# Performance work log

Hardware: AMD Instinct MI355X
Metric: run time of the kernel (lower is better)

## Reference

```python
import jax, jax.numpy as jnp
import numpy as np

N = 25000      # nodes per type
E = 300000     # weight-edge rows
K = 16         # neighbors
F = 64         # in_feat
A = 64         # atten_dim
DW = 64        # weight_dim
CB = 8         # num_bit_conv
CV = 8         # num_vector_conv
OUT = 64       # out_feat
IN_K = CB * F + CV * (3 + 2 + 1)


def setup_inputs() -> dict:
    key = jax.random.key(0)
    ks = jax.random.split(key, 40)
    s = 0.05
    d = {}
    d['eu'] = jax.random.normal(ks[0], (N, F), jnp.float32)
    d['ei'] = jax.random.normal(ks[1], (N, F), jnp.float32)
    d['et'] = jax.random.normal(ks[2], (N, F), jnp.float32)
    d['ew'] = jax.random.normal(ks[3], (E, DW), jnp.float32)
    names = ['u_iw_j', 'u_tw_j', 'i_uw_j', 'i_tw_j', 't_uw_j', 't_iw_j']
    for i, nm in enumerate(names):
        d[nm] = jax.random.randint(ks[4 + i], (N, K), 0, N, jnp.int64 if jax.config.jax_enable_x64 else jnp.int32)
        d[nm.replace('_j', '_w')] = jax.random.randint(ks[10 + i], (N, K), 0, E, jnp.int64 if jax.config.jax_enable_x64 else jnp.int32)
    # per-type Attention1 params: user, item, tag
    for i, t in enumerate(['user', 'item', 'tag']):
        b = 16 + 4 * i
        d[f'W1_{t}'] = jax.random.normal(ks[b], (F + DW, A), jnp.float32) * s
        d[f'W2_{t}'] = jax.random.normal(ks[b + 1], (F, A), jnp.float32) * s
        d[f'b_{t}'] = jax.random.normal(ks[b + 2], (1, A), jnp.float32) * s
        d[f'v_{t}'] = jax.random.normal(ks[b + 3], (1, A), jnp.float32) * s
    d['U'] = jax.random.normal(ks[28], (F, A), jnp.float32) * s
    d['q'] = jax.random.normal(ks[29], (1, A), jnp.float32) * s
    d['p'] = jax.random.normal(ks[30], (1, A), jnp.float32) * s
    d['W_bit'] = jax.random.normal(ks[31], (CB, 3), jnp.float32) * s       # Conv2d(1,CB,(3,1))
    d['W_vec1'] = jax.random.normal(ks[32], (CV, 1, F), jnp.float32) * s   # Conv2d(1,CV,(1,F))
    d['W_vec2'] = jax.random.normal(ks[33], (CV, 2, F), jnp.float32) * s
    d['W_vec3'] = jax.random.normal(ks[34], (CV, 3, F), jnp.float32) * s
    d['Wf'] = jax.random.normal(ks[35], (IN_K, OUT), jnp.float32) * s
    d['bf'] = jax.random.normal(ks[36], (1, OUT), jnp.float32) * s
    return d


def _atten1(ev, ej, ew, v_j, v_w, W1, W2, b, v):
    ejp = jnp.concatenate([jnp.zeros((1, ej.shape[1]), ej.dtype), ej], axis=0)
    ewp = jnp.concatenate([jnp.zeros((1, ew.shape[1]), ew.dtype), ew], axis=0)
    eNj = ejp[v_j]                                  # [N,K,F]
    eNw = ewp[v_w]                                  # [N,K,DW]
    eNv = jnp.broadcast_to(ev[:, None, :], (ev.shape[0], v_j.shape[1], ev.shape[1]))
    eN_vw = jnp.concatenate([eNv, eNw], axis=-1)    # [N,K,F+DW]
    av = jnp.einsum('nkd,da->nka', eN_vw, W1) + jnp.einsum('nkf,fa->nka', eNj, W2) + b
    x = jax.nn.relu(av) @ v.T                       # [N,K,1]
    a = jax.nn.softmax(x, axis=1)
    return jnp.sum(a * eNj, axis=1)                 # [N,F]


def _atten2(u, i, t, U, q, p):
    uit = jnp.stack([u, i, t], axis=1)              # [N,3,F]
    x = jnp.einsum('nsf,fa->nsa', uit, U) + q
    x = jax.nn.relu(x) @ p.T                        # [N,3,1]
    b = jax.nn.softmax(x, axis=1)
    return b * uit                                  # [N,3,F]


def _conv(eN, W_bit, W_vec1, W_vec2, W_vec3):
    # eN: [N,3,F]
    bit = jax.nn.relu(jnp.einsum('njf,cj->ncf', eN, W_bit))       # [N,CB,F]
    bit = bit.reshape(bit.shape[0], -1)
    vec = []
    for j, W in ((1, W_vec1), (2, W_vec2), (3, W_vec3)):
        win = jnp.stack([eN[:, s:s + j, :] for s in range(3 - j + 1)], axis=1)  # [N,4-j,j,F]
        y = jax.nn.relu(jnp.einsum('nsjf,cjf->ncs', win, W))       # [N,CV,4-j]
        vec.append(y.reshape(y.shape[0], -1))
    return jnp.concatenate([bit] + vec, axis=1)                    # [N,IN_K]


def _forward(eu, ei, et, ew, params, idx):
    (W1u, W2u, bu, vu, W1i, W2i, bi, vi, W1t, W2t, bt, vt,
     U, q, p, W_bit, W_vec1, W_vec2, W_vec3, Wf, bf) = params
    (u_iw_j, u_iw_w, u_tw_j, u_tw_w, i_uw_j, i_uw_w,
     i_tw_j, i_tw_w, t_uw_j, t_uw_w, t_iw_j, t_iw_w) = idx
    eu_iN = _atten1(eu, ei, ew, u_iw_j, u_iw_w, W1i, W2i, bi, vi)
    eu_tN = _atten1(eu, et, ew, u_tw_j, u_tw_w, W1t, W2t, bt, vt)
    ei_uN = _atten1(ei, eu, ew, i_uw_j, i_uw_w, W1u, W2u, bu, vu)
    ei_tN = _atten1(ei, et, ew, i_tw_j, i_tw_w, W1t, W2t, bt, vt)
    et_uN = _atten1(et, eu, ew, t_uw_j, t_uw_w, W1u, W2u, bu, vu)
    et_iN = _atten1(et, ei, ew, t_iw_j, t_iw_w, W1i, W2i, bi, vi)
    euN = _atten2(eu, eu_iN, eu_tN, U, q, p)
    eiN = _atten2(ei_uN, ei, ei_tN, U, q, p)
    etN = _atten2(et_uN, et_iN, et, U, q, p)
    out = []
    for eN in (euN, eiN, etN):
        c = _conv(eN, W_bit, W_vec1, W_vec2, W_vec3)
        out.append(jax.nn.relu(c @ Wf + bf))
    return tuple(out)


def reference(eu, ei, et, ew,
              u_iw_j, u_iw_w, u_tw_j, u_tw_w, i_uw_j, i_uw_w, i_tw_j, i_tw_w,
              t_uw_j, t_uw_w, t_iw_j, t_iw_w,
              W1_user, W2_user, b_user, v_user,
              W1_item, W2_item, b_item, v_item,
              W1_tag, W2_tag, b_tag, v_tag,
              U, q, p, W_bit, W_vec1, W_vec2, W_vec3, Wf, bf):
    params = (W1_user, W2_user, b_user, v_user, W1_item, W2_item, b_item, v_item,
              W1_tag, W2_tag, b_tag, v_tag, U, q, p, W_bit, W_vec1, W_vec2, W_vec3, Wf, bf)
    idx = (u_iw_j, u_iw_w, u_tw_j, u_tw_w, i_uw_j, i_uw_w,
           i_tw_j, i_tw_w, t_uw_j, t_uw_w, t_iw_j, t_iw_w)
    return _forward(eu, ei, et, ew, params, idx)
```

## Files before the change

### kernel.cpp

```cpp
#include <hip/hip_runtime.h>
#include <math.h>

#define NN 25000
#define EE 300000
#define NT 1563
#define ET128 2344
#define NT128 196

typedef __attribute__((ext_vector_type(8))) short bf16x8;
typedef __attribute__((ext_vector_type(4))) float f32x4;
typedef __attribute__((ext_vector_type(2))) float f32x2;
typedef __attribute__((ext_vector_type(2))) __fp16 h2;

__device__ __forceinline__ unsigned short f2bf(float f) {
    union { float f; unsigned u; } a; a.f = f;
    unsigned r = (a.u + 0x7fffu + ((a.u >> 16) & 1u)) >> 16;
    return (unsigned short)r;
}
__device__ __forceinline__ unsigned pack2(float lo, float hi) {
    return (unsigned)f2bf(lo) | ((unsigned)f2bf(hi) << 16);
}
__device__ __forceinline__ float bflo(unsigned p) {
    union { unsigned u; float f; } a; a.u = p << 16; return a.f;
}
__device__ __forceinline__ float bfhi(unsigned p) {
    union { unsigned u; float f; } a; a.u = p & 0xffff0000u; return a.f;
}
__device__ __forceinline__ unsigned packfp8x4(float a, float b, float c, float d) {
    int v = __builtin_amdgcn_cvt_pk_fp8_f32(a, b, 0, 0);
    v = __builtin_amdgcn_cvt_pk_fp8_f32(c, d, v, 1);
    return (unsigned)v;
}
__device__ __forceinline__ unsigned pkh(float lo, float hi) {
    h2 r = __builtin_amdgcn_cvt_pkrtz(lo, hi);
    return __builtin_bit_cast(unsigned, r);
}
template<bool HI>
__device__ __forceinline__ h2 fp8toh(unsigned v) {
#if __has_builtin(__builtin_amdgcn_cvt_scalef32_pk_f16_fp8)
    return __builtin_amdgcn_cvt_scalef32_pk_f16_fp8((int)v, 1.0f, HI);
#else
    f32x2 f = __builtin_amdgcn_cvt_pk_f32_fp8((int)v, HI);
    return __builtin_amdgcn_cvt_pkrtz(f.x, f.y);
#endif
}
__device__ __forceinline__ float hdot(h2 a, h2 b, float c) {
#if __has_builtin(__builtin_amdgcn_fdot2)
    return __builtin_amdgcn_fdot2(a, b, c, false);
#else
    return c + (float)a[0] * (float)b[0] + (float)a[1] * (float)b[1];
#endif
}
__device__ __forceinline__ h2 hmax0(h2 a) {
    h2 z; z[0] = (__fp16)0.f; z[1] = (__fp16)0.f;
#if __has_builtin(__builtin_elementwise_max)
    return __builtin_elementwise_max(a, z);
#else
    h2 r;
    r[0] = a[0] > z[0] ? a[0] : z[0];
    r[1] = a[1] > z[1] ? a[1] : z[1];
    return r;
#endif
}

__global__ __launch_bounds__(256) void head_kernel(
    const float* __restrict__ ew,
    const float* __restrict__ eu, const float* __restrict__ ei, const float* __restrict__ et,
    const float* __restrict__ W1u, const float* __restrict__ W1i, const float* __restrict__ W1t,
    const float* __restrict__ W2u, const float* __restrict__ W2i, const float* __restrict__ W2t,
    const float* __restrict__ bu, const float* __restrict__ bi, const float* __restrict__ bt,
    unsigned char* __restrict__ gw8, unsigned* __restrict__ preB,
    unsigned char* __restrict__ JG)
{
    __shared__ __align__(16) unsigned short stA[64 * 72];
    __shared__ __align__(16) float cSa[64 * 68];
    __shared__ __align__(16) float cSb[64 * 68];
    const int t = threadIdx.x;
    const int lane = t & 63, wv = t >> 6;
    const int l15 = lane & 15, quad = lane >> 4;
    const int cw = wv * 16 + l15;
    const int bx = blockIdx.x;

    if (bx < ET128) {
        if (bx == 0 && t < 48) {
            int w = t >> 4;
            ((unsigned*)(gw8 + (size_t)w * (EE + 1) * 64))[t & 15] = 0u;
        }
        const float* Ws[3] = { W1u + 4096, W1i + 4096, W1t + 4096 };
        bf16x8 bf[3][2];
        #pragma unroll
        for (int w = 0; w < 3; ++w)
            #pragma unroll
            for (int ks = 0; ks < 2; ++ks)
                #pragma unroll
                for (int j = 0; j < 8; ++j)
                    bf[w][ks][j] = (short)f2bf(Ws[w][(ks * 32 + quad * 8 + j) * 64 + cw]);

        #pragma unroll
        for (int tile = 0; tile < 2; ++tile) {
            const int rowBase = bx * 128 + tile * 64;
            #pragma unroll
            for (int i = 0; i < 4; ++i) {
                int idx = t + i * 256;
                int row = idx >> 4, cg = idx & 15;
                int gr = rowBase + row;
                float4 v4 = (gr < EE) ? *(const float4*)(ew + (size_t)gr * 64 + cg * 4)
                                      : make_float4(0.f, 0.f, 0.f, 0.f);
                uint2 pk = { pack2(v4.x, v4.y), pack2(v4.z, v4.w) };
                *(uint2*)&stA[row * 72 + cg * 4] = pk;
            }
            __syncthreads();
            bf16x8 af[4][2];
            #pragma unroll
            for (int m = 0; m < 4; ++m)
                #pragma unroll
                for (int ks = 0; ks < 2; ++ks)
                    af[m][ks] = *(const bf16x8*)&stA[(m * 16 + l15) * 72 + ks * 32 + quad * 8];

            f32x4 acc[3][4];
            #pragma unroll
            for (int w = 0; w < 3; ++w)
                #pragma unroll
                for (int m = 0; m < 4; ++m) {
                    acc[w][m].x = 0; acc[w][m].y = 0; acc[w][m].z = 0; acc[w][m].w = 0;
                    #pragma unroll
                    for (int ks = 0; ks < 2; ++ks)
                        acc[w][m] = __builtin_amdgcn_mfma_f32_16x16x32_bf16(af[m][ks], bf[w][ks], acc[w][m], 0, 0, 0);
                }

            #define EG_WRITE(BUF, W) {                                               \
                _Pragma("unroll")                                                    \
                for (int m = 0; m < 4; ++m)                                          \
                    _Pragma("unroll")                                                \
                    for (int r = 0; r < 4; ++r)                                      \
                        BUF[(m * 16 + quad * 4 + r) * 68 + cw] = acc[W][m][r];       \
            }
            #define EG_STORE(BUF, W) {                                               \
                unsigned char* outg = gw8 + (size_t)(W) * (EE + 1) * 64 + 64;        \
                _Pragma("unroll")                                                    \
                for (int i = 0; i < 2; ++i) {                                        \
                    int task = t + i * 256;                                          \
                    int row = task >> 3, seg = task & 7;                             \
                    int gr = rowBase + row;                                          \
                    if (gr < EE) {                                                   \
                        float4 a = *(const float4*)&BUF[row * 68 + seg * 8];         \
                        float4 b = *(const float4*)&BUF[row * 68 + seg * 8 + 4];     \
                        uint2 pk = { packfp8x4(a.x, a.y, a.z, a.w),                  \
                                     packfp8x4(b.x, b.y, b.z, b.w) };                \
                        *(uint2*)(outg + (size_t)gr * 64 + seg * 8) = pk;            \
                    }                                                                \
                }                                                                    \
            }
            EG_WRITE(cSa, 0);
            __syncthreads();
            EG_STORE(cSa, 0);
            EG_WRITE(cSb, 1);
            __syncthreads();
            EG_STORE(cSb, 1);
            EG_WRITE(cSa, 2);
            __syncthreads();
            EG_STORE(cSa, 2);
            #undef EG_WRITE
            #undef EG_STORE
        }
    } else {
        const int yy = bx - ET128;
        const int y = yy / NT128;
        const int rowBase0 = (yy - y * NT128) * 128;
        if (rowBase0 == 0 && t < 48)
            ((unsigned*)(JG + (size_t)y * (NN + 1) * 192))[t] = 0u;
        const float* X; const float* Wa; const float* Wb; const float* W2;
        const float* ba; const float* bb; int oa, ob;
        switch (y) {
            case 0:  X = eu; Wa = W1i; ba = bi; oa = 0; Wb = W1t; bb = bt; ob = 1; W2 = W2u; break;
            case 1:  X = ei; Wa = W1u; ba = bu; oa = 2; Wb = W1t; bb = bt; ob = 3; W2 = W2i; break;
            default: X = et; Wa = W1u; ba = bu; oa = 4; Wb = W1i; bb = bi; ob = 5; W2 = W2t; break;
        }
        const float* Ws[3] = { Wa, Wb, W2 };
        const float bias_cw[3] = { ba[cw], bb[cw], 0.f };
        bf16x8 bf[3][2];
        #pragma unroll
        for (int w = 0; w < 3; ++w)
            #pragma unroll
            for (int ks = 0; ks < 2; ++ks)
                #pragma unroll
                for (int j = 0; j < 8; ++j)
                    bf[w][ks][j] = (short)f2bf(Ws[w][(ks * 32 + quad * 8 + j) * 64 + cw]);

        #pragma unroll
        for (int tile = 0; tile < 2; ++tile) {
            const int rowBase = rowBase0 + tile * 64;
            if (tile) __syncthreads();
            #pragma unroll
            for (int i = 0; i < 4; ++i) {
                int idx = t + i * 256;
                int row = idx >> 4, cg = idx & 15;
                int gr = rowBase + row;
                float4 v4 = (gr < NN) ? *(const float4*)(X + (size_t)gr * 64 + cg * 4)
                                      : make_float4(0.f, 0.f, 0.f, 0.f);
                uint2 pk = { pack2(v4.x, v4.y), pack2(v4.z, v4.w) };
                *(uint2*)&stA[row * 72 + cg * 4] = pk;
            }
            __syncthreads();
            bf16x8 af[4][2];
            #pragma unroll
            for (int m = 0; m < 4; ++m)
                #pragma unroll
                for (int ks = 0; ks < 2; ++ks)
                    af[m][ks] = *(const bf16x8*)&stA[(m * 16 + l15) * 72 + ks * 32 + quad * 8];

            f32x4 acc[3][4];
            #pragma unroll
            for (int w = 0; w < 3; ++w)
                #pragma unroll
                for (int m = 0; m < 4; ++m) {
                    acc[w][m].x = 0; acc[w][m].y = 0; acc[w][m].z = 0; acc[w][m].w = 0;
                    #pragma unroll
                    for (int ks = 0; ks < 2; ++ks)
                        acc[w][m] = __builtin_amdgcn_mfma_f32_16x16x32_bf16(af[m][ks], bf[w][ks], acc[w][m], 0, 0, 0);
                }

            #define NG_WRITE(BUF, W) {                                                     \
                _Pragma("unroll")                                                          \
                for (int m = 0; m < 4; ++m)                                                \
                    _Pragma("unroll")                                                      \
                    for (int r = 0; r < 4; ++r)                                            \
                        BUF[(m * 16 + quad * 4 + r) * 68 + cw] = acc[W][m][r] + bias_cw[W];\
            }
            #define NG_STORE(BUF, W) {                                                     \
                _Pragma("unroll")                                                          \
                for (int i = 0; i < 2; ++i) {                                              \
                    int task = t + i * 256;                                                \
                    int row = task >> 3, seg = task & 7;                                   \
                    int gr = rowBase + row;                                                \
                    if (gr < NN) {                                                         \
                        float4 a = *(const float4*)&BUF[row * 68 + seg * 8];               \
                        float4 b = *(const float4*)&BUF[row * 68 + seg * 8 + 4];           \
                        if ((W) < 2) {                                                     \
                            int oi = ((W) == 0) ? oa : ob;                                 \
                            uint4 pk = { pkh(a.x, a.y), pkh(a.z, a.w),                     \
                                         pkh(b.x, b.y), pkh(b.z, b.w) };                   \
                            *(uint4*)(preB + ((size_t)oi * NN + gr) * 32 + seg * 4) = pk;  \
                        } else {                                                           \
                            unsigned char* dst = JG + ((size_t)y * (NN + 1) + gr + 1) * 192;\
                            uint2 gj = { packfp8x4(a.x, a.y, a.z, a.w),                    \
                                         packfp8x4(b.x, b.y, b.z, b.w) };                  \
                            *(uint2*)(dst + seg * 8) = gj;                                 \
                            uint4 ej = *(const uint4*)&stA[row * 72 + seg * 8];            \
                            *(uint4*)(dst + 64 + seg * 16) = ej;                           \
                        }                                                                  \
                    }                                                                      \
                }                                                                          \
            }
            NG_WRITE(cSa, 0);
            __syncthreads();
            NG_STORE(cSa, 0);
            NG_WRITE(cSb, 1);
            __syncthreads();
            NG_STORE(cSb, 1);
            NG_WRITE(cSa, 2);
            __syncthreads();
            NG_STORE(cSa, 2);
            #undef NG_WRITE
            #undef NG_STORE
        }
    }
}

__global__ __launch_bounds__(256) void atten1_kernel(
    const unsigned* __restrict__ preB, const unsigned char* __restrict__ gw8,
    const unsigned char* __restrict__ JG,
    const float* __restrict__ vu, const float* __restrict__ vi, const float* __restrict__ vt,
    const int* __restrict__ u_iw_j, const int* __restrict__ u_iw_w,
    const int* __restrict__ u_tw_j, const int* __restrict__ u_tw_w,
    const int* __restrict__ i_uw_j, const int* __restrict__ i_uw_w,
    const int* __restrict__ i_tw_j, const int* __restrict__ i_tw_w,
    const int* __restrict__ t_uw_j, const int* __restrict__ t_uw_w,
    const int* __restrict__ t_iw_j, const int* __restrict__ t_iw_w,
    unsigned* __restrict__ aoB)
{
    const int g = blockIdx.y;
    const int p = blockIdx.x & 1;
    const int tile = blockIdx.x >> 1;
    int y; const int* Vj; const int* Vw;
    switch (g * 2 + p) {
        case 0:  y = 2; Vj = i_uw_j; Vw = i_uw_w; break;
        case 1:  y = 4; Vj = t_uw_j; Vw = t_uw_w; break;
        case 2:  y = 0; Vj = u_iw_j; Vw = u_iw_w; break;
        case 3:  y = 5; Vj = t_iw_j; Vw = t_iw_w; break;
        case 4:  y = 1; Vj = u_tw_j; Vw = u_tw_w; break;
        default: y = 3; Vj = i_tw_j; Vw = i_tw_w; break;
    }
    const float* v = (g == 0) ? vu : (g == 1) ? vi : vt;
    const unsigned* pre = preB + (size_t)y * NN * 32;
    const unsigned char* gw = gw8 + (size_t)g * (EE + 1) * 64;
    const unsigned char* jg = JG + (size_t)g * (NN + 1) * 192;
    unsigned*            out = aoB + (size_t)y * NN * 32;

    const int lane = threadIdx.x & 63;
    const int n = tile * 4 + (threadIdx.x >> 6);
    const int q = lane >> 4, r = lane & 15;

    const uint2 prep = *(const uint2*)(pre + (size_t)n * 32 + 2 * r);
    const h2 pre01 = __builtin_bit_cast(h2, prep.x);
    const h2 pre23 = __builtin_bit_cast(h2, prep.y);
    const float4 v4 = *(const float4*)(v + r * 4);
    const h2 v01h = __builtin_amdgcn_cvt_pkrtz(v4.x, v4.y);
    const h2 v23h = __builtin_amdgcn_cvt_pkrtz(v4.z, v4.w);

    const int4 wi = *(const int4*)(Vw + n * 16 + q * 4);
    const int4 ji = *(const int4*)(Vj + n * 16 + q * 4);
    const int wid[4] = { wi.x, wi.y, wi.z, wi.w };
    const int jid[4] = { ji.x, ji.y, ji.z, ji.w };

    unsigned gwv[4], gjv[4]; uint2 ejv[4];
    #pragma unroll
    for (int i = 0; i < 4; ++i)
        gwv[i] = *(const unsigned*)(gw + (size_t)wid[i] * 64 + r * 4);
    #pragma unroll
    for (int i = 0; i < 4; ++i) {
        const unsigned char* row = jg + (size_t)jid[i] * 192;
        gjv[i] = *(const unsigned*)(row + r * 4);
        ejv[i] = *(const uint2*)(row + 64 + r * 8);
    }

    float xk[4];
    #pragma unroll
    for (int i = 0; i < 4; ++i) {
        h2 g01 = fp8toh<false>(gwv[i]);
        h2 g23 = fp8toh<true>(gwv[i]);
        h2 j01 = fp8toh<false>(gjv[i]);
        h2 j23 = fp8toh<true>(gjv[i]);
        h2 z01 = hmax0(pre01 + g01 + j01);
        h2 z23 = hmax0(pre23 + g23 + j23);
        float x = hdot(z01, v01h, 0.f);
        x = hdot(z23, v23h, x);
        x += __shfl_xor(x, 1, 64);
        x += __shfl_xor(x, 2, 64);
        x += __shfl_xor(x, 4, 64);
        x += __shfl_xor(x, 8, 64);
        xk[i] = x;
    }
    float m = fmaxf(fmaxf(xk[0], xk[1]), fmaxf(xk[2], xk[3]));
    m = fmaxf(m, __shfl_xor(m, 16, 64));
    m = fmaxf(m, __shfl_xor(m, 32, 64));
    float e0 = __expf(xk[0] - m), e1 = __expf(xk[1] - m);
    float e2 = __expf(xk[2] - m), e3 = __expf(xk[3] - m);
    float s = (e0 + e1) + (e2 + e3);
    s += __shfl_xor(s, 16, 64);
    s += __shfl_xor(s, 32, 64);
    const float inv = 1.f / s;

    const float wgt[4] = { e0 * inv, e1 * inv, e2 * inv, e3 * inv };
    f32x2 A01; A01.x = 0.f; A01.y = 0.f;
    f32x2 A23; A23.x = 0.f; A23.y = 0.f;
    #pragma unroll
    for (int i = 0; i < 4; ++i) {
        f32x2 w2; w2.x = wgt[i]; w2.y = wgt[i];
        f32x2 e01; e01.x = bflo(ejv[i].x); e01.y = bfhi(ejv[i].x);
        f32x2 e23; e23.x = bflo(ejv[i].y); e23.y = bfhi(ejv[i].y);
        A01 = e01 * w2 + A01;
        A23 = e23 * w2 + A23;
    }
    float a0 = A01.x, a1 = A01.y, a2 = A23.x, a3 = A23.y;
    a0 += __shfl_xor(a0, 16, 64); a0 += __shfl_xor(a0, 32, 64);
    a1 += __shfl_xor(a1, 16, 64); a1 += __shfl_xor(a1, 32, 64);
    a2 += __shfl_xor(a2, 16, 64); a2 += __shfl_xor(a2, 32, 64);
    a3 += __shfl_xor(a3, 16, 64); a3 += __shfl_xor(a3, 32, 64);
    if (q == 0) {
        uint2 pk = { pack2(a0, a1), pack2(a2, a3) };
        *(uint2*)(out + (size_t)n * 32 + 2 * r) = pk;
    }
}

__global__ __launch_bounds__(256, 3) void tail_kernel(
    const float* __restrict__ eu, const float* __restrict__ ei, const float* __restrict__ et,
    const unsigned* __restrict__ aoB,
    const float* __restrict__ U, const float* __restrict__ q, const float* __restrict__ p,
    const float* __restrict__ Wbit, const float* __restrict__ Wv1,
    const float* __restrict__ Wv2, const float* __restrict__ Wv3,
    const float* __restrict__ Wf, const float* __restrict__ bfv,
    float* __restrict__ out)
{
    __shared__ __align__(16) unsigned short uitA[48 * 72];
    __shared__ __align__(16) unsigned short eNA[48 * 72];
    __shared__ __align__(16) unsigned short wcf[6 * 64 * 8];
    __shared__ __align__(16) unsigned short c_sh[16 * 584];
    __shared__ float G_sh[48 * 52];
    __shared__ float xpart[4 * 48];
    __shared__ float bcoef[16 * 4];

    const int t = threadIdx.x;
    const int lane = t & 63;
    const int wv = t >> 6;
    const int l15 = lane & 15;
    const int quad = lane >> 4;
    const int type = blockIdx.y;
    const float* xf = (type == 0) ? eu : (type == 1) ? ei : et;
    const int cw = wv * 16 + l15;
    const float qv = q[cw], pv = p[cw], bfb = bfv[cw];

    float wb[8][3];
    #pragma unroll
    for (int c = 0; c < 8; ++c)
        #pragma unroll
        for (int s = 0; s < 3; ++s) wb[c][s] = Wbit[c * 3 + s];

    bf16x8 ufrag[2];
    #pragma unroll
    for (int ks = 0; ks < 2; ++ks)
        #pragma unroll
        for (int j = 0; j < 8; ++j) {
            int f = ks * 32 + quad * 8 + j;
            ufrag[ks][j] = (short)f2bf(U[f * 64 + cw]);
        }
    bf16x8 wff[18];
    #pragma unroll
    for (int ks = 0; ks < 18; ++ks)
        #pragma unroll
        for (int j = 0; j < 8; ++j) {
            int k = ks * 32 + quad * 8 + j;
            float w = (k < 560) ? Wf[(size_t)k * 64 + cw] : 0.f;
            wff[ks][j] = (short)f2bf(w);
        }
    for (int slot = t; slot < 384; slot += 256) {
        int fi = slot >> 6, l = slot & 63;
        int nt_ = fi >> 1, ks = fi & 1;
        int r = nt_ * 16 + (l & 15);
        unsigned short vals[8];
        #pragma unroll
        for (int j = 0; j < 8; ++j) {
            int f = ks * 32 + (l >> 4) * 8 + j;
            float wv_;
            if (r < 8)       wv_ = Wv1[r * 64 + f];
            else if (r < 24) { int u = r - 8;  wv_ = Wv2[(u >> 1) * 128 + (u & 1) * 64 + f]; }
            else             { int u = r - 24; wv_ = Wv3[(u / 3) * 192 + (u % 3) * 64 + f]; }
            vals[j] = f2bf(wv_);
        }
        uint4 pk = { (unsigned)vals[0] | ((unsigned)vals[1] << 16),
                     (unsigned)vals[2] | ((unsigned)vals[3] << 16),
                     (unsigned)vals[4] | ((unsigned)vals[5] << 16),
                     (unsigned)vals[6] | ((unsigned)vals[7] << 16) };
        *(uint4*)&wcf[slot * 8] = pk;
    }

    for (int tile = blockIdx.x; tile < NT; tile += gridDim.x) {
        const int nodeBase = tile * 16;
        __syncthreads();
        #pragma unroll
        for (int i = 0; i < 3; ++i) {
            int idx = t + i * 256;
            int row = idx >> 4, cg = idx & 15;
            int nl = row / 3, s = row - nl * 3;
            int n = nodeBase + nl;
            uint2 pk;
            if (s == type) {
                float4 v4 = (n < NN) ? *(const float4*)(xf + (size_t)n * 64 + cg * 4)
                                     : make_float4(0.f, 0.f, 0.f, 0.f);
                pk.x = pack2(v4.x, v4.y); pk.y = pack2(v4.z, v4.w);
            } else {
                int aoidx = (type == 0) ? (s - 1)
                          : (type == 1) ? ((s == 0) ? 2 : 3)
                                        : ((s == 0) ? 4 : 5);
                pk = (n < NN) ? *(const uint2*)(aoB + ((size_t)aoidx * NN + n) * 32 + cg * 2)
                              : make_uint2(0u, 0u);
            }
            *(uint2*)&uitA[row * 72 + cg * 4] = pk;
        }
        __syncthreads();
        {
            f32x4 av[3];
            #pragma unroll
            for (int mt = 0; mt < 3; ++mt) { av[mt].x = 0; av[mt].y = 0; av[mt].z = 0; av[mt].w = 0; }
            #pragma unroll
            for (int mt = 0; mt < 3; ++mt)
                #pragma unroll
                for (int ks = 0; ks < 2; ++ks) {
                    bf16x8 a = *(const bf16x8*)&uitA[(mt * 16 + l15) * 72 + ks * 32 + quad * 8];
                    av[mt] = __builtin_amdgcn_mfma_f32_16x16x32_bf16(a, ufrag[ks], av[mt], 0, 0, 0);
                }
            #pragma unroll
            for (int mt = 0; mt < 3; ++mt)
                #pragma unroll
                for (int r = 0; r < 4; ++r) {
                    float val = fmaxf(av[mt][r] + qv, 0.f) * pv;
                    val += __shfl_xor(val, 1, 64); val += __shfl_xor(val, 2, 64);
                    val += __shfl_xor(val, 4, 64); val += __shfl_xor(val, 8, 64);
                    if (l15 == 0) xpart[wv * 48 + mt * 16 + quad * 4 + r] = val;
                }
        }
        __syncthreads();
        if (t < 16) {
            float xv[3];
            #pragma unroll
            for (int s = 0; s < 3; ++s)
                xv[s] = xpart[t * 3 + s] + xpart[48 + t * 3 + s]
                      + xpart[96 + t * 3 + s] + xpart[144 + t * 3 + s];
            float mm = fmaxf(xv[0], fmaxf(xv[1], xv[2]));
            float e0 = __expf(xv[0] - mm), e1 = __expf(xv[1] - mm), e2 = __expf(xv[2] - mm);
            float inv = 1.f / (e0 + e1 + e2);
            bcoef[t * 4 + 0] = e0 * inv; bcoef[t * 4 + 1] = e1 * inv; bcoef[t * 4 + 2] = e2 * inv;
        }
        __syncthreads();
        #pragma unroll
        for (int i = 0; i < 2; ++i) {
            int task = t + i * 256;
            int nl = task >> 5, fp = task & 31;
            float b0 = bcoef[nl * 4], b1 = bcoef[nl * 4 + 1], b2 = bcoef[nl * 4 + 2];
            unsigned u0 = *(const unsigned*)&uitA[(nl * 3 + 0) * 72 + fp * 2];
            unsigned u1 = *(const unsigned*)&uitA[(nl * 3 + 1) * 72 + fp * 2];
            unsigned u2 = *(const unsigned*)&uitA[(nl * 3 + 2) * 72 + fp * 2];
            float e0l = b0 * bflo(u0), e0h = b0 * bfhi(u0);
            float e1l = b1 * bflo(u1), e1h = b1 * bfhi(u1);
            float e2l = b2 * bflo(u2), e2h = b2 * bfhi(u2);
            *(unsigned*)&eNA[(nl * 3 + 0) * 72 + fp * 2] = pack2(e0l, e0h);
            *(unsigned*)&eNA[(nl * 3 + 1) * 72 + fp * 2] = pack2(e1l, e1h);
            *(unsigned*)&eNA[(nl * 3 + 2) * 72 + fp * 2] = pack2(e2l, e2h);
            #pragma unroll
            for (int c = 0; c < 8; ++c) {
                float lo = fmaxf(wb[c][0] * e0l + wb[c][1] * e1l + wb[c][2] * e2l, 0.f);
                float hi = fmaxf(wb[c][0] * e0h + wb[c][1] * e1h + wb[c][2] * e2h, 0.f);
                *(unsigned*)&c_sh[nl * 584 + c * 64 + fp * 2] = pack2(lo, hi);
            }
        }
        __syncthreads();
        #pragma unroll
        for (int pi = 0; pi < 3; ++pi) {
            int pr = wv + pi * 4;
            if (pr < 9) {
                int mm = pr / 3, nn_ = pr - mm * 3;
                f32x4 g; g.x = 0; g.y = 0; g.z = 0; g.w = 0;
                #pragma unroll
                for (int ks = 0; ks < 2; ++ks) {
                    bf16x8 a = *(const bf16x8*)&eNA[(mm * 16 + l15) * 72 + ks * 32 + quad * 8];
                    bf16x8 b = *(const bf16x8*)&wcf[((nn_ * 2 + ks) * 64 + lane) * 8];
                    g = __builtin_amdgcn_mfma_f32_16x16x32_bf16(a, b, g, 0, 0, 0);
                }
                #pragma unroll
                for (int r = 0; r < 4; ++r)
                    G_sh[(mm * 16 + quad * 4 + r) * 52 + nn_ * 16 + l15] = g[r];
            }
        }
        __syncthreads();
        #pragma unroll
        for (int i = 0; i < 4; ++i) {
            int task = t + i * 256;
            int vvv = task >> 4, nl = task & 15;
            unsigned short res = 0;
            if (vvv < 24) {
                int c = vvv / 3, s = vvv - c * 3;
                res = f2bf(fmaxf(G_sh[(nl * 3 + s) * 52 + c], 0.f));
            } else if (vvv < 40) {
                int u = vvv - 24, c = u >> 1, s = u & 1;
                float val = G_sh[(nl * 3 + s) * 52 + 8 + 2 * c]
                          + G_sh[(nl * 3 + s + 1) * 52 + 8 + 2 * c + 1];
                res = f2bf(fmaxf(val, 0.f));
            } else if (vvv < 48) {
                int c = vvv - 40;
                float val = G_sh[(nl * 3 + 0) * 52 + 24 + 3 * c]
                          + G_sh[(nl * 3 + 1) * 52 + 24 + 3 * c + 1]
                          + G_sh[(nl * 3 + 2) * 52 + 24 + 3 * c + 2];
                res = f2bf(fmaxf(val, 0.f));
            }
            c_sh[nl * 584 + 512 + vvv] = res;
        }
        __syncthreads();
        {
            f32x4 acc; acc.x = 0; acc.y = 0; acc.z = 0; acc.w = 0;
            const unsigned short* ap = &c_sh[l15 * 584 + quad * 8];
            #pragma unroll
            for (int ks = 0; ks < 18; ++ks) {
                bf16x8 a = *(const bf16x8*)(ap + ks * 32);
                acc = __builtin_amdgcn_mfma_f32_16x16x32_bf16(a, wff[ks], acc, 0, 0, 0);
            }
            float* outT = out + (size_t)type * NN * 64;
            #pragma unroll
            for (int r = 0; r < 4; ++r) {
                int node = nodeBase + quad * 4 + r;
                if (node < NN) outT[(size_t)node * 64 + cw] = fmaxf(acc[r] + bfb, 0.f);
            }
        }
    }
}

extern "C" void kernel_launch(void* const* d_in, const int* in_sizes, int n_in,
                              void* d_out, int out_size, void* d_ws, size_t ws_size,
                              hipStream_t stream)
{
    const float* eu = (const float*)d_in[0];
    const float* ei = (const float*)d_in[1];
    const float* et = (const float*)d_in[2];
    const float* ew = (const float*)d_in[3];
    const int* u_iw_j = (const int*)d_in[4];
    const int* u_iw_w = (const int*)d_in[5];
    const int* u_tw_j = (const int*)d_in[6];
    const int* u_tw_w = (const int*)d_in[7];
    const int* i_uw_j = (const int*)d_in[8];
    const int* i_uw_w = (const int*)d_in[9];
    const int* i_tw_j = (const int*)d_in[10];
    const int* i_tw_w = (const int*)d_in[11];
    const int* t_uw_j = (const int*)d_in[12];
    const int* t_uw_w = (const int*)d_in[13];
    const int* t_iw_j = (const int*)d_in[14];
    const int* t_iw_w = (const int*)d_in[15];
    const float* W1_user = (const float*)d_in[16];
    const float* W2_user = (const float*)d_in[17];
    const float* b_user  = (const float*)d_in[18];
    const float* v_user  = (const float*)d_in[19];
    const float* W1_item = (const float*)d_in[20];
    const float* W2_item = (const float*)d_in[21];
    const float* b_item  = (const float*)d_in[22];
    const float* v_item  = (const float*)d_in[23];
    const float* W1_tag  = (const float*)d_in[24];
    const float* W2_tag  = (const float*)d_in[25];
    const float* b_tag   = (const float*)d_in[26];
    const float* v_tag   = (const float*)d_in[27];
    const float* U    = (const float*)d_in[28];
    const float* q    = (const float*)d_in[29];
    const float* p    = (const float*)d_in[30];
    const float* Wbit = (const float*)d_in[31];
    const float* Wv1  = (const float*)d_in[32];
    const float* Wv2  = (const float*)d_in[33];
    const float* Wv3  = (const float*)d_in[34];
    const float* Wf   = (const float*)d_in[35];
    const float* bfv  = (const float*)d_in[36];
    float* out = (float*)d_out;

    unsigned char* gw8 = (unsigned char*)d_ws;
    unsigned* preB = (unsigned*)(gw8 + (size_t)3 * (EE + 1) * 64);
    unsigned char* JG = (unsigned char*)(preB + (size_t)6 * NN * 32);
    unsigned* aoB = (unsigned*)(JG + (size_t)3 * (NN + 1) * 192);

    const dim3 blk(256);

    head_kernel<<<ET128 + 3 * NT128, blk, 0, stream>>>(
        ew, eu, ei, et,
        W1_user, W1_item, W1_tag, W2_user, W2_item, W2_tag,
        b_user, b_item, b_tag, gw8, preB, JG);

    atten1_kernel<<<dim3(2 * (NN / 4), 3), blk, 0, stream>>>(
        preB, gw8, JG, v_user, v_item, v_tag,
        u_iw_j, u_iw_w, u_tw_j, u_tw_w, i_uw_j, i_uw_w,
        i_tw_j, i_tw_w, t_uw_j, t_uw_w, t_iw_j, t_iw_w, aoB);

    tail_kernel<<<dim3(256, 3), blk, 0, stream>>>(
        eu, ei, et, aoB,
        U, q, p, Wbit, Wv1, Wv2, Wv3, Wf, bfv, out);
}
```

Baseline: 390.3 us.

## Compute neighbor W2 projection on the fly with MFMA in atten1 instead of precomputing

The head kernel no longer precomputes the fp8 W2 projection for every node, and stores only the bf16 neighbor embeddings (128 B per row instead of 192 B). An extra head block packs the W2 weights into MFMA fragment layout. atten1 now gathers the bf16 neighbor rows and runs two MFMA ops per 16-column tile to form ej@W2 for all 16 neighbors at once, with permuted output layouts for gw8 and preB to match the MFMA result mapping. This removes one GEMM output pass and shrinks gathered bytes, at the cost of extra MFMA work per edge and a different lane-to-neighbor mapping with more shuffles.

Result: slower. 428.6 us (+9.8%).

```diff
diff --git a/kernel.cpp b/kernel.cpp
--- a/kernel.cpp
+++ b/kernel.cpp
@@ -25,6 +25,9 @@
 }
 __device__ __forceinline__ float bfhi(unsigned p) {
     union { unsigned u; float f; } a; a.u = p & 0xffff0000u; return a.f;
+}
+__device__ __forceinline__ float bfs(short s) {
+    union { unsigned u; float f; } a; a.u = ((unsigned)(unsigned short)s) << 16; return a.f;
 }
 __device__ __forceinline__ unsigned packfp8x4(float a, float b, float c, float d) {
     int v = __builtin_amdgcn_cvt_pk_fp8_f32(a, b, 0, 0);
@@ -70,7 +73,7 @@
     const float* __restrict__ W2u, const float* __restrict__ W2i, const float* __restrict__ W2t,
     const float* __restrict__ bu, const float* __restrict__ bi, const float* __restrict__ bt,
     unsigned char* __restrict__ gw8, unsigned* __restrict__ preB,
-    unsigned char* __restrict__ JG)
+    unsigned char* __restrict__ ejB, unsigned short* __restrict__ wfrag)
 {
     __shared__ __align__(16) unsigned short stA[64 * 72];
     __shared__ __align__(16) float cSa[64 * 68];
@@ -143,8 +146,11 @@
                     int row = task >> 3, seg = task & 7;                             \
                     int gr = rowBase + row;                                          \
                     if (gr < EE) {                                                   \
-                        float4 a = *(const float4*)&BUF[row * 68 + seg * 8];         \
-                        float4 b = *(const float4*)&BUF[row * 68 + seg * 8 + 4];     \
+                        int d0 = seg * 2, d1 = seg * 2 + 1;                          \
+                        int f0a = (d0 & 3) * 16 + (d0 >> 2) * 4;                     \
+                        int f0b = (d1 & 3) * 16 + (d1 >> 2) * 4;                     \
+                        float4 a = *(const float4*)&BUF[row * 68 + f0a];             \
+                        float4 b = *(const float4*)&BUF[row * 68 + f0b];             \
                         uint2 pk = { packfp8x4(a.x, a.y, a.z, a.w),                  \
                                      packfp8x4(b.x, b.y, b.z, b.w) };                \
                         *(uint2*)(outg + (size_t)gr * 64 + seg * 8) = pk;            \
@@ -163,24 +169,25 @@
             #undef EG_WRITE
             #undef EG_STORE
         }
-    } else {
+    } else if (bx < ET128 + 3 * NT128) {
         const int yy = bx - ET128;
         const int y = yy / NT128;
         const int rowBase0 = (yy - y * NT128) * 128;
-        if (rowBase0 == 0 && t < 48)
-            ((unsigned*)(JG + (size_t)y * (NN + 1) * 192))[t] = 0u;
-        const float* X; const float* Wa; const float* Wb; const float* W2;
+        if (rowBase0 == 0 && t < 32)
+            ((unsigned*)(ejB + (size_t)y * (NN + 1) * 128))[t] = 0u;
+        const float* X; const float* Wa; const float* Wb;
         const float* ba; const float* bb; int oa, ob;
         switch (y) {
-            case 0:  X = eu; Wa = W1i; ba = bi; oa = 0; Wb = W1t; bb = bt; ob = 1; W2 = W2u; break;
-            case 1:  X = ei; Wa = W1u; ba = bu; oa = 2; Wb = W1t; bb = bt; ob = 3; W2 = W2i; break;
-            default: X = et; Wa = W1u; ba = bu; oa = 4; Wb = W1i; bb = bi; ob = 5; W2 = W2t; break;
-        }
-        const float* Ws[3] = { Wa, Wb, W2 };
-        const float bias_cw[3] = { ba[cw], bb[cw], 0.f };
-        bf16x8 bf[3][2];
-        #pragma unroll
-        for (int w = 0; w < 3; ++w)
+            case 0:  X = eu; Wa = W1i; ba = bi; oa = 0; Wb = W1t; bb = bt; ob = 1; break;
+            case 1:  X = ei; Wa = W1u; ba = bu; oa = 2; Wb = W1t; bb = bt; ob = 3; break;
+            default: X = et; Wa = W1u; ba = bu; oa = 4; Wb = W1i; bb = bi; ob = 5; break;
+        }
+        const float* Ws[2] = { Wa, Wb };
+        const float bias_cw[2] = { ba[cw], bb[cw] };
+        const int oi_[2] = { oa, ob };
+        bf16x8 bf[2][2];
+        #pragma unroll
+        for (int w = 0; w < 2; ++w)
             #pragma unroll
             for (int ks = 0; ks < 2; ++ks)
                 #pragma unroll
@@ -190,7 +197,6 @@
         #pragma unroll
         for (int tile = 0; tile < 2; ++tile) {
             const int rowBase = rowBase0 + tile * 64;
-            if (tile) __syncthreads();
             #pragma unroll
             for (int i = 0; i < 4; ++i) {
                 int idx = t + i * 256;
@@ -209,9 +215,9 @@
                 for (int ks = 0; ks < 2; ++ks)
                     af[m][ks] = *(const bf16x8*)&stA[(m * 16 + l15) * 72 + ks * 32 + quad * 8];
 
-            f32x4 acc[3][4];
-            #pragma unroll
-            for (int w = 0; w < 3; ++w)
+            f32x4 acc[2][4];
+            #pragma unroll
+            for (int w = 0; w < 2; ++w)
                 #pragma unroll
                 for (int m = 0; m < 4; ++m) {
                     acc[w][m].x = 0; acc[w][m].y = 0; acc[w][m].z = 0; acc[w][m].w = 0;
@@ -227,49 +233,68 @@
                     for (int r = 0; r < 4; ++r)                                            \
                         BUF[(m * 16 + quad * 4 + r) * 68 + cw] = acc[W][m][r] + bias_cw[W];\
             }
-            #define NG_STORE(BUF, W) {                                                     \
+            #define NG_STORE_PRE(BUF, W) {                                                 \
                 _Pragma("unroll")                                                          \
                 for (int i = 0; i < 2; ++i) {                                              \
                     int task = t + i * 256;                                                \
                     int row = task >> 3, seg = task & 7;                                   \
                     int gr = rowBase + row;                                                \
                     if (gr < NN) {                                                         \
-                        float4 a = *(const float4*)&BUF[row * 68 + seg * 8];               \
-                        float4 b = *(const float4*)&BUF[row * 68 + seg * 8 + 4];           \
-                        if ((W) < 2) {                                                     \
-                            int oi = ((W) == 0) ? oa : ob;                                 \
-                            uint4 pk = { pkh(a.x, a.y), pkh(a.z, a.w),                     \
-                                         pkh(b.x, b.y), pkh(b.z, b.w) };                   \
-                            *(uint4*)(preB + ((size_t)oi * NN + gr) * 32 + seg * 4) = pk;  \
-                        } else {                                                           \
-                            unsigned char* dst = JG + ((size_t)y * (NN + 1) + gr + 1) * 192;\
-                            uint2 gj = { packfp8x4(a.x, a.y, a.z, a.w),                    \
-                                         packfp8x4(b.x, b.y, b.z, b.w) };                  \
-                            *(uint2*)(dst + seg * 8) = gj;                                 \
-                            uint4 ej = *(const uint4*)&stA[row * 72 + seg * 8];            \
-                            *(uint4*)(dst + 64 + seg * 16) = ej;                           \
+                        unsigned uu[4];                                                    \
+                        _Pragma("unroll")                                                  \
+                        for (int cu = 0; cu < 4; ++cu) {                                   \
+                            int u = seg * 4 + cu;                                          \
+                            int f = ((u >> 1) & 3) * 16 + (u >> 3) * 4 + 2 * (u & 1);      \
+                            uu[cu] = pkh(BUF[row * 68 + f], BUF[row * 68 + f + 1]);        \
                         }                                                                  \
+                        uint4 pk = { uu[0], uu[1], uu[2], uu[3] };                         \
+                        *(uint4*)(preB + ((size_t)oi_[W] * NN + gr) * 32 + seg * 4) = pk;  \
                     }                                                                      \
                 }                                                                          \
             }
             NG_WRITE(cSa, 0);
             __syncthreads();
-            NG_STORE(cSa, 0);
+            NG_STORE_PRE(cSa, 0);
+            #pragma unroll
+            for (int i = 0; i < 2; ++i) {
+                int task = t + i * 256;
+                int row = task >> 3, seg = task & 7;
+                int gr = rowBase + row;
+                if (gr < NN)
+                    *(uint4*)(ejB + ((size_t)y * (NN + 1) + gr + 1) * 128 + seg * 16) =
+                        *(const uint4*)&stA[row * 72 + seg * 8];
+            }
             NG_WRITE(cSb, 1);
             __syncthreads();
-            NG_STORE(cSb, 1);
-            NG_WRITE(cSa, 2);
-            __syncthreads();
-            NG_STORE(cSa, 2);
+            NG_STORE_PRE(cSb, 1);
             #undef NG_WRITE
-            #undef NG_STORE
+            #undef NG_STORE_PRE
+        }
+    } else {
+        const float* W2s[3] = { W2u, W2i, W2t };
+        #pragma unroll
+        for (int it = 0; it < 6; ++it) {
+            int idx = t + it * 256;
+            int fg = idx >> 6, ll = idx & 63;
+            int gg = fg >> 3, mt = (fg >> 1) & 3, ks = fg & 1;
+            int l15_ = ll & 15, quad_ = ll >> 4;
+            const float* W2 = W2s[gg];
+            unsigned short vals[8];
+            #pragma unroll
+            for (int j = 0; j < 8; ++j)
+                vals[j] = f2bf(W2[(ks * 32 + quad_ * 8 + j) * 64 + mt * 16 + l15_]);
+            uint4 pk = { (unsigned)vals[0] | ((unsigned)vals[1] << 16),
+                         (unsigned)vals[2] | ((unsigned)vals[3] << 16),
+                         (unsigned)vals[4] | ((unsigned)vals[5] << 16),
+                         (unsigned)vals[6] | ((unsigned)vals[7] << 16) };
+            *(uint4*)(wfrag + (size_t)(fg * 64 + ll) * 8) = pk;
         }
     }
 }
 
 __global__ __launch_bounds__(256) void atten1_kernel(
     const unsigned* __restrict__ preB, const unsigned char* __restrict__ gw8,
-    const unsigned char* __restrict__ JG,
+    const unsigned char* __restrict__ ejB, const unsigned short* __restrict__ wfrag,
     const float* __restrict__ vu, const float* __restrict__ vi, const float* __restrict__ vt,
     const int* __restrict__ u_iw_j, const int* __restrict__ u_iw_w,
     const int* __restrict__ u_tw_j, const int* __restrict__ u_tw_w,
@@ -294,82 +319,91 @@
     const float* v = (g == 0) ? vu : (g == 1) ? vi : vt;
     const unsigned* pre = preB + (size_t)y * NN * 32;
     const unsigned char* gw = gw8 + (size_t)g * (EE + 1) * 64;
-    const unsigned char* jg = JG + (size_t)g * (NN + 1) * 192;
+    const unsigned char* ejp = ejB + (size_t)g * (NN + 1) * 128;
+    const bf16x8* wf = (const bf16x8*)(wfrag + (size_t)g * 8 * 64 * 8);
     unsigned*            out = aoB + (size_t)y * NN * 32;
 
     const int lane = threadIdx.x & 63;
     const int n = tile * 4 + (threadIdx.x >> 6);
-    const int q = lane >> 4, r = lane & 15;
-
-    const uint2 prep = *(const uint2*)(pre + (size_t)n * 32 + 2 * r);
-    const h2 pre01 = __builtin_bit_cast(h2, prep.x);
-    const h2 pre23 = __builtin_bit_cast(h2, prep.y);
-    const float4 v4 = *(const float4*)(v + r * 4);
-    const h2 v01h = __builtin_amdgcn_cvt_pkrtz(v4.x, v4.y);
-    const h2 v23h = __builtin_amdgcn_cvt_pkrtz(v4.z, v4.w);
-
-    const int4 wi = *(const int4*)(Vw + n * 16 + q * 4);
-    const int4 ji = *(const int4*)(Vj + n * 16 + q * 4);
-    const int wid[4] = { wi.x, wi.y, wi.z, wi.w };
-    const int jid[4] = { ji.x, ji.y, ji.z, ji.w };
-
-    unsigned gwv[4], gjv[4]; uint2 ejv[4];
+    const int l15 = lane & 15, quad = lane >> 4;
+
+    const int wid = Vw[n * 16 + l15];
+    const int jid = Vj[n * 16 + l15];
+
+    const uint4 gwv = *(const uint4*)(gw + (size_t)wid * 64 + quad * 16);
+    const bf16x8 bfr0 = *(const bf16x8*)(ejp + (size_t)jid * 128 + quad * 16);
+    const bf16x8 bfr1 = *(const bf16x8*)(ejp + (size_t)jid * 128 + 64 + quad * 16);
+    const uint4 ph0 = *(const uint4*)(pre + (size_t)n * 32 + quad * 8);
+    const uint4 ph1 = *(const uint4*)(pre + (size_t)n * 32 + quad * 8 + 4);
+    const unsigned pu[8] = { ph0.x, ph0.y, ph0.z, ph0.w, ph1.x, ph1.y, ph1.z, ph1.w };
+    const unsigned ga[4] = { gwv.x, gwv.y, gwv.z, gwv.w };
+
+    h2 vp01[4], vp23[4];
     #pragma unroll
-    for (int i = 0; i < 4; ++i)
-        gwv[i] = *(const unsigned*)(gw + (size_t)wid[i] * 64 + r * 4);
+    for (int mt = 0; mt < 4; ++mt) {
+        float4 vv = *(const float4*)(v + mt * 16 + quad * 4);
+        vp01[mt] = __builtin_amdgcn_cvt_pkrtz(vv.x, vv.y);
+        vp23[mt] = __builtin_amdgcn_cvt_pkrtz(vv.z, vv.w);
+    }
+
+    float x = 0.f;
     #pragma unroll
-    for (int i = 0; i < 4; ++i) {
-        const unsigned char* row = jg + (size_t)jid[i] * 192;
-        gjv[i] = *(const unsigned*)(row + r * 4);
-        ejv[i] = *(const uint2*)(row + 64 + r * 8);
-    }
-
-    float xk[4];
+    for (int mt = 0; mt < 4; ++mt) {
+        bf16x8 a0 = wf[(mt * 2 + 0) * 64 + lane];
+        bf16x8 a1 = wf[(mt * 2 + 1) * 64 + lane];
+        f32x4 c; c.x = 0; c.y = 0; c.z = 0; c.w = 0;
+        c = __builtin_amdgcn_mfma_f32_16x16x32_bf16(a0, bfr0, c, 0, 0, 0);
+        c = __builtin_amdgcn_mfma_f32_16x16x32_bf16(a1, bfr1, c, 0, 0, 0);
+        h2 g01 = fp8toh<false>(ga[mt]);
+        h2 g23 = fp8toh<true>(ga[mt]);
+        h2 p01 = __builtin_bit_cast(h2, pu[mt * 2]);
+        h2 p23 = __builtin_bit_cast(h2, pu[mt * 2 + 1]);
+        h2 j01 = __builtin_amdgcn_cvt_pkrtz(c.x, c.y);
+        h2 j23 = __builtin_amdgcn_cvt_pkrtz(c.z, c.w);
+        h2 z01 = hmax0(p01 + g01 + j01);
+        h2 z23 = hmax0(p23 + g23 + j23);
+        x = hdot(z01, vp01[mt], x);
+        x = hdot(z23, vp23[mt], x);
+    }
+    x += __shfl_xor(x, 16, 64);
+    x += __shfl_xor(x, 32, 64);
+
+    float m = x;
+    m = fmaxf(m, __shfl_xor(m, 1, 64));
+    m = fmaxf(m, __shfl_xor(m, 2, 64));
+    m = fmaxf(m, __shfl_xor(m, 4, 64));
+    m = fmaxf(m, __shfl_xor(m, 8, 64));
+    float e = __expf(x - m);
+    float s = e;
+    s += __shfl_xor(s, 1, 64);
+    s += __shfl_xor(s, 2, 64);
+    s += __shfl_xor(s, 4, 64);
+    s += __shfl_xor(s, 8, 64);
+    const float w = e * (1.f / s);
+
+    f32x2 ac[8];
     #pragma unroll
-    for (int i = 0; i < 4; ++i) {
-        h2 g01 = fp8toh<false>(gwv[i]);
-        h2 g23 = fp8toh<true>(gwv[i]);
-        h2 j01 = fp8toh<false>(gjv[i]);
-        h2 j23 = fp8toh<true>(gjv[i]);
-        h2 z01 = hmax0(pre01 + g01 + j01);
-        h2 z23 = hmax0(pre23 + g23 + j23);
-        float x = hdot(z01, v01h, 0.f);
-        x = hdot(z23, v23h, x);
-        x += __shfl_xor(x, 1, 64);
-        x += __shfl_xor(x, 2, 64);
-        x += __shfl_xor(x, 4, 64);
-        x += __shfl_xor(x, 8, 64);
-        xk[i] = x;
-    }
-    float m = fmaxf(fmaxf(xk[0], xk[1]), fmaxf(xk[2], xk[3]));
-    m = fmaxf(m, __shfl_xor(m, 16, 64));
-    m = fmaxf(m, __shfl_xor(m, 32, 64));
-    float e0 = __expf(xk[0] - m), e1 = __expf(xk[1] - m);
-    float e2 = __expf(xk[2] - m), e3 = __expf(xk[3] - m);
-    float s = (e0 + e1) + (e2 + e3);
-    s += __shfl_xor(s, 16, 64);
-    s += __shfl_xor(s, 32, 64);
-    const float inv = 1.f / s;
-
-    const float wgt[4] = { e0 * inv, e1 * inv, e2 * inv, e3 * inv };
-    f32x2 A01; A01.x = 0.f; A01.y = 0.f;
-    f32x2 A23; A23.x = 0.f; A23.y = 0.f;
+    for (int jp = 0; jp < 4; ++jp) {
+        f32x2 e0; e0.x = bfs(bfr0[2 * jp]); e0.y = bfs(bfr0[2 * jp + 1]);
+        f32x2 e1; e1.x = bfs(bfr1[2 * jp]); e1.y = bfs(bfr1[2 * jp + 1]);
+        f32x2 w2; w2.x = w; w2.y = w;
+        ac[jp] = e0 * w2;
+        ac[4 + jp] = e1 * w2;
+    }
     #pragma unroll
-    for (int i = 0; i < 4; ++i) {
-        f32x2 w2; w2.x = wgt[i]; w2.y = wgt[i];
-        f32x2 e01; e01.x = bflo(ejv[i].x); e01.y = bfhi(ejv[i].x);
-        f32x2 e23; e23.x = bflo(ejv[i].y); e23.y = bfhi(ejv[i].y);
-        A01 = e01 * w2 + A01;
-        A23 = e23 * w2 + A23;
-    }
-    float a0 = A01.x, a1 = A01.y, a2 = A23.x, a3 = A23.y;
-    a0 += __shfl_xor(a0, 16, 64); a0 += __shfl_xor(a0, 32, 64);
-    a1 += __shfl_xor(a1, 16, 64); a1 += __shfl_xor(a1, 32, 64);
-    a2 += __shfl_xor(a2, 16, 64); a2 += __shfl_xor(a2, 32, 64);
-    a3 += __shfl_xor(a3, 16, 64); a3 += __shfl_xor(a3, 32, 64);
-    if (q == 0) {
-        uint2 pk = { pack2(a0, a1), pack2(a2, a3) };
-        *(uint2*)(out + (size_t)n * 32 + 2 * r) = pk;
+    for (int st = 1; st <= 8; st <<= 1)
+        #pragma unroll
+        for (int i = 0; i < 8; ++i) {
+            ac[i].x += __shfl_xor(ac[i].x, st, 64);
+            ac[i].y += __shfl_xor(ac[i].y, st, 64);
+        }
+    if (l15 == 0) {
+        uint4 o0 = { pack2(ac[0].x, ac[0].y), pack2(ac[1].x, ac[1].y),
+                     pack2(ac[2].x, ac[2].y), pack2(ac[3].x, ac[3].y) };
+        uint4 o1 = { pack2(ac[4].x, ac[4].y), pack2(ac[5].x, ac[5].y),
+                     pack2(ac[6].x, ac[6].y), pack2(ac[7].x, ac[7].y) };
+        *(uint4*)(out + (size_t)n * 32 + quad * 4) = o0;
+        *(uint4*)(out + (size_t)n * 32 + 16 + quad * 4) = o1;
     }
 }
 
@@ -628,18 +662,19 @@
 
     unsigned char* gw8 = (unsigned char*)d_ws;
     unsigned* preB = (unsigned*)(gw8 + (size_t)3 * (EE + 1) * 64);
-    unsigned char* JG = (unsigned char*)(preB + (size_t)6 * NN * 32);
-    unsigned* aoB = (unsigned*)(JG + (size_t)3 * (NN + 1) * 192);
+    unsigned char* ejB = (unsigned char*)(preB + (size_t)6 * NN * 32);
+    unsigned* aoB = (unsigned*)(ejB + (size_t)3 * (NN + 1) * 128);
+    unsigned short* wfrag = (unsigned short*)(aoB + (size_t)6 * NN * 32);
 
     const dim3 blk(256);
 
-    head_kernel<<<ET128 + 3 * NT128, blk, 0, stream>>>(
+    head_kernel<<<ET128 + 3 * NT128 + 1, blk, 0, stream>>>(
         ew, eu, ei, et,
         W1_user, W1_item, W1_tag, W2_user, W2_item, W2_tag,
-        b_user, b_item, b_tag, gw8, preB, JG);
+        b_user, b_item, b_tag, gw8, preB, ejB, wfrag);
 
     atten1_kernel<<<dim3(2 * (NN / 4), 3), blk, 0, stream>>>(
-        preB, gw8, JG, v_user, v_item, v_tag,
+        preB, gw8, ejB, wfrag, v_user, v_item, v_tag,
         u_iw_j, u_iw_w, u_tw_j, u_tw_w, i_uw_j, i_uw_w,
         i_tw_j, i_tw_w, t_uw_j, t_uw_w, t_iw_j, t_iw_w, aoB);
 
```
